# Performance work log

Hardware: AMD Instinct MI355X
Metric: run time of the kernel (lower is better)

Reference implementation:

```python
import jax, jax.numpy as jnp
import numpy as np

B, S, D, H, HID = 8192, 16, 128, 8, 1024
DH = D // H  # 16
GCN, NUMF = 40, 103
EPS = 1e-5

def _make_pe():
    pos = np.arange(S, dtype=np.float64)[:, None]
    i = np.arange(D, dtype=np.float64)[None, :]
    pe = pos / np.power(10000.0, (i // 2 * 2.0) / D)
    pe[:, 0::2] = np.sin(pe[:, 0::2])
    pe[:, 1::2] = np.cos(pe[:, 1::2])
    return jnp.asarray(pe, dtype=jnp.float32)  # [S, D]

PE = _make_pe()

def setup_inputs() -> dict:
    key = jax.random.key(0)
    ks = jax.random.split(key, 16)
    rn = lambda k, shape, s=0.02: (jax.random.normal(k, shape, jnp.float32) * s)
    return {
        "x": jax.random.normal(ks[0], (B, S, D), jnp.float32),
        "gcn_i": jax.random.normal(ks[1], (B, GCN), jnp.float32),
        "num": jax.random.normal(ks[2], (B, NUMF), jnp.float32),
        # two independent encoder layers, params stacked on leading dim
        "Wq": rn(ks[3], (2, D, D)), "bq": jnp.zeros((2, D), jnp.float32),
        "Wk": rn(ks[4], (2, D, D)), "bk": jnp.zeros((2, D), jnp.float32),
        "Wv": rn(ks[5], (2, D, D)), "bv": jnp.zeros((2, D), jnp.float32),
        "Wo": rn(ks[6], (2, D, D)), "bo": jnp.zeros((2, D), jnp.float32),
        "ln1_g": jnp.ones((2, D), jnp.float32), "ln1_b": jnp.zeros((2, D), jnp.float32),
        "W1": rn(ks[7], (2, D, HID)), "b1": jnp.zeros((2, HID), jnp.float32),
        "W2": rn(ks[8], (2, HID, D)), "b2": jnp.zeros((2, D), jnp.float32),
        "ln2_g": jnp.ones((2, D), jnp.float32), "ln2_b": jnp.zeros((2, D), jnp.float32),
        # head
        "Wn": rn(ks[9], (NUMF, D)), "bnum": jnp.zeros((D,), jnp.float32),
        "bn_gamma": jnp.ones((D,), jnp.float32), "bn_beta": jnp.zeros((D,), jnp.float32),
        "Wf": rn(ks[10], (S * D + GCN + D, 1)), "bf": jnp.zeros((1,), jnp.float32),
    }

def _ln(x, g, b):
    m = x.mean(-1, keepdims=True)
    v = ((x - m) ** 2).mean(-1, keepdims=True)
    return (x - m) * jax.lax.rsqrt(v + EPS) * g + b

def reference(x, gcn_i, num, Wq, bq, Wk, bk, Wv, bv, Wo, bo, ln1_g, ln1_b,
              W1, b1, W2, b2, ln2_g, ln2_b, Wn, bnum, bn_gamma, bn_beta, Wf, bf):
    out = x + PE  # positional encoding (dropout = identity in eval)
    scale = DH ** -0.5
    for l in range(2):
        # NOTE: original uses a raw .view(B*H, -1, DH) (no transpose) -- faithful reshape
        q = (out @ Wq[l] + bq[l]).reshape(B * H, S, DH)
        k = (out @ Wk[l] + bk[l]).reshape(B * H, S, DH)
        v = (out @ Wv[l] + bv[l]).reshape(B * H, S, DH)
        attn = jax.nn.softmax(jnp.einsum('nsd,ntd->nst', q, k) * scale, axis=-1)
        ctx = jnp.einsum('nst,ntd->nsd', attn, v).reshape(B, S, D)
        h = _ln(ctx @ Wo[l] + bo[l] + out, ln1_g[l], ln1_b[l])
        ff = jax.nn.relu(h @ W1[l] + b1[l]) @ W2[l] + b2[l]
        out = _ln(ff + h, ln2_g[l], ln2_b[l])
    flat = out.reshape(B, S * D)  # [B, 2048]
    n = num @ Wn + bnum  # [B, 128]
    # BatchNorm1d, training-mode forward (biased batch variance)
    mu = n.mean(0)
    var = ((n - mu) ** 2).mean(0)
    n = (n - mu) * jax.lax.rsqrt(var + EPS) * bn_gamma + bn_beta
    p = jnp.concatenate([flat, gcn_i, n], axis=-1)  # [B, 2216]
    return jax.nn.sigmoid(p @ Wf + bf)
```

## Files before the change

### kernel.cpp

```cpp
#include <hip/hip_runtime.h>
#include <hip/hip_bf16.h>
#include <math.h>

#define B_SZ   8192
#define S_SZ   16
#define D_SZ   128
#define HID_SZ 1024
#define NUMF_SZ 103
#define GCN_SZ 40
#define G_B    4
#define NBLK   (B_SZ / G_B)
#define SBLK   512
#define STRD   136

typedef short bh8 __attribute__((ext_vector_type(8)));
typedef float fx4 __attribute__((ext_vector_type(4)));
typedef unsigned short us4 __attribute__((ext_vector_type(4)));

__device__ __forceinline__ fx4 mfma16(bh8 a, bh8 b, fx4 c) {
    return __builtin_amdgcn_mfma_f32_16x16x32_bf16(a, b, c, 0, 0, 0);
}

__device__ __forceinline__ unsigned short f2b(float f) {
    union { __hip_bfloat16 b; unsigned short u; } cv;
    cv.b = __float2bfloat16(f);
    return cv.u;
}
__device__ __forceinline__ float bu2f(unsigned short u) {
    return __uint_as_float(((unsigned)u) << 16);
}

__global__ __launch_bounds__(256) void prep_weights(
    const float* __restrict__ Wq, const float* __restrict__ Wk,
    const float* __restrict__ Wv, const float* __restrict__ Wo,
    const float* __restrict__ W1, const float* __restrict__ W2,
    unsigned short* __restrict__ WswQ, unsigned short* __restrict__ WswK,
    unsigned short* __restrict__ WswV, unsigned short* __restrict__ WswO,
    unsigned short* __restrict__ Wsw1, unsigned short* __restrict__ Wsw2,
    float* __restrict__ PEt)
{
    int j = blockIdx.x * 256 + threadIdx.x;
    if (j < 2048) {
        int s = j >> 7, c = j & 127;
        float expo = (float)((c >> 1) * 2) * (1.0f / 128.0f);
        float denom = powf(10000.0f, expo);
        float ang = (float)s / denom;
        PEt[j] = (c & 1) ? cosf(ang) : sinf(ang);
    }
    if (j < 2 * 16384) {
        int r = j & 16383, l = j >> 14;
        int k = r >> 7, n = r & 127;
        int dst = (((l * 8 + (n >> 4)) * 4 + (k >> 5)) * 64 +
                   (((k >> 3) & 3) * 16 + (n & 15))) * 8 + (k & 7);
        WswQ[dst] = f2b(Wq[j]); WswK[dst] = f2b(Wk[j]);
        WswV[dst] = f2b(Wv[j]); WswO[dst] = f2b(Wo[j]);
    }
    {
        int l = j >> 17, r = j & 131071;
        int k = r >> 10, n = r & 1023;
        int dst = (((l * 64 + (n >> 4)) * 4 + (k >> 5)) * 64 +
                   (((k >> 3) & 3) * 16 + (n & 15))) * 8 + (k & 7);
        Wsw1[dst] = f2b(W1[j]);
    }
    {
        int l = j >> 17, r = j & 131071;
        int k = r >> 7, n = r & 127;
        int dst = (((l * 8 + (n >> 4)) * 32 + (k >> 5)) * 64 +
                   (((k >> 3) & 3) * 16 + (n & 15))) * 8 + (k & 7);
        Wsw2[dst] = f2b(W2[j]);
    }
}

__global__ __launch_bounds__(256, 2) void encoder_fused(
    const float* __restrict__ x, const float* __restrict__ gcn,
    const float* __restrict__ bq, const float* __restrict__ bk,
    const float* __restrict__ bv, const float* __restrict__ bo,
    const float* __restrict__ ln1g, const float* __restrict__ ln1b,
    const float* __restrict__ b1, const float* __restrict__ b2p,
    const float* __restrict__ ln2g, const float* __restrict__ ln2b,
    const float* __restrict__ Wf,
    const unsigned short* __restrict__ WswQ, const unsigned short* __restrict__ WswK,
    const unsigned short* __restrict__ WswV, const unsigned short* __restrict__ WswO,
    const unsigned short* __restrict__ Wsw1, const unsigned short* __restrict__ Wsw2,
    const float* __restrict__ PEt,
    const float* __restrict__ num, const float* __restrict__ Wn,
    const float* __restrict__ bnum,
    float* __restrict__ ssum, float* __restrict__ ssq,
    unsigned int* __restrict__ cnt,
    const float* __restrict__ bng, const float* __restrict__ bnb,
    const float* __restrict__ bfin, float* __restrict__ cvec,
    float* __restrict__ acc1)
{
    __shared__ unsigned short ACT[64][STRD];
    __shared__ unsigned short Qb[64][STRD];
    __shared__ unsigned short Kb[64][STRD];
    __shared__ unsigned short Vb[64][STRD];
    __shared__ float2 LNp2[64][4];
    __shared__ unsigned short Pb[4][16][16];
    __shared__ int lastf;

    unsigned short* Vb4 = &Vb[0][0];

    const int t = threadIdx.x;
    const int w = t >> 6, lane = t & 63;
    const int q = lane >> 4, ln = lane & 15;

    if (blockIdx.x < SBLK) {
        float* NUMs = (float*)ACT;
        float* cred = (float*)Qb;
        float* cS   = (float*)Vb;
        float* redw = (float*)LNp2;
        const int b0 = blockIdx.x * 16;
        const int j = t & 127, sg = t >> 7, s0 = sg * 8;

        for (int idx = t; idx < 16 * NUMF_SZ; idx += 256) {
            int r = idx / NUMF_SZ, f = idx - r * NUMF_SZ;
            NUMs[r * 104 + f] = num[(size_t)(b0 + r) * NUMF_SZ + f];
        }
        __syncthreads();

        float acc[8];
        float bnv = bnum[j];
#pragma unroll
        for (int r = 0; r < 8; ++r) acc[r] = bnv;
        for (int f = 0; f < NUMF_SZ; ++f) {
            float wv = Wn[f * 128 + j];
#pragma unroll
            for (int r = 0; r < 8; ++r) acc[r] = fmaf(NUMs[(s0 + r) * 104 + f], wv, acc[r]);
        }
        float lsum = 0.f, lsq = 0.f;
#pragma unroll
        for (int r = 0; r < 8; ++r) {
            lsum += acc[r];
            lsq = fmaf(acc[r], acc[r], lsq);
        }
        cred[sg * 128 + j] = lsum;
        cred[(2 + sg) * 128 + j] = lsq;
        __syncthreads();
        if (sg == 0) atomicAdd(&ssum[j], cred[j] + cred[128 + j]);
        else         atomicAdd(&ssq[j],  cred[256 + j] + cred[384 + j]);
        __syncthreads();
        if (t == 0) lastf = (atomicAdd(cnt, 1u) == SBLK - 1u) ? 1 : 0;
        __syncthreads();

        if (lastf) {
            float C1p = 0.f;
            if (t < 128) {
                float sv = atomicAdd(&ssum[t], 0.f);
                float qv = atomicAdd(&ssq[t], 0.f);
                float mean = sv * (1.0f / (float)B_SZ);
                float var = qv * (1.0f / (float)B_SZ) - mean * mean;
                float inv = rsqrtf(var + 1e-5f);
                float wj = Wf[2088 + t];
                float gi = bng[t] * inv;
                float cj = gi * wj;
                cS[t] = cj;
                C1p = (bnb[t] - mean * gi) * wj + bnum[t] * cj;
            }
#pragma unroll
            for (int o = 32; o; o >>= 1) C1p += __shfl_xor(C1p, o);
            if (lane == 0) redw[w] = C1p;
            __syncthreads();
            if (t == 0) cvec[103] = redw[0] + redw[1] + redw[2] + redw[3] + bfin[0];
            if (t < NUMF_SZ) {
                float s2 = 0.f;
                for (int jj = 0; jj < 128; ++jj)
                    s2 = fmaf(Wn[t * 128 + jj], cS[jj], s2);
                cvec[t] = s2;
            }
        }
        return;
    }

    const int bbase = (blockIdx.x - SBLK) * G_B;

    {
        const float4* xb = (const float4*)(x + (size_t)bbase * 2048);
        const float4* pe4 = (const float4*)PEt;
#pragma unroll
        for (int i = 0; i < 8; ++i) {
            int f4 = i * 256 + t;
            float4 xv = xb[f4];
            float4 pv = pe4[f4 & 511];
            int flat = f4 * 4;
            int row = flat >> 7, col = flat & 127;
            ushort4 pk = {f2b(xv.x + pv.x), f2b(xv.y + pv.y),
                          f2b(xv.z + pv.z), f2b(xv.w + pv.w)};
            *(ushort4*)&ACT[row][col] = pk;
        }
    }
    __syncthreads();

    for (int l = 0; l < 2; ++l) {
        {
            bh8 afr[4][4];
#pragma unroll
            for (int mt = 0; mt < 4; ++mt)
#pragma unroll
                for (int ks = 0; ks < 4; ++ks)
                    afr[mt][ks] = *(const bh8*)&ACT[mt * 16 + ln][ks * 32 + q * 8];
#pragma unroll
            for (int mtx = 0; mtx < 2; ++mtx) {
                const unsigned short* Wm = (mtx == 0) ? WswQ + l * 16384 : WswK + l * 16384;
                const float* bias = (mtx == 0) ? bq + l * 128 : bk + l * 128;
                unsigned short (*dst)[STRD] = (mtx == 0) ? Qb : Kb;
#pragma unroll
                for (int i2 = 0; i2 < 2; ++i2) {
                    int nt = w * 2 + i2;
                    bh8 wfr[4];
#pragma unroll
                    for (int ks = 0; ks < 4; ++ks)
                        wfr[ks] = *(const bh8*)(Wm + ((nt * 4 + ks) * 64 + lane) * 8);
                    int n0 = nt * 16 + q * 4;
                    fx4 bb4 = *(const fx4*)&bias[n0];
#pragma unroll
                    for (int mt = 0; mt < 4; ++mt) {
                        fx4 acc = {0.f, 0.f, 0.f, 0.f};
#pragma unroll
                        for (int ks = 0; ks < 4; ++ks) acc = mfma16(wfr[ks], afr[mt][ks], acc);
                        us4 o;
#pragma unroll
                        for (int r2 = 0; r2 < 4; ++r2) o[r2] = f2b(acc[r2] + bb4[r2]);
                        *(us4*)&dst[mt * 16 + ln][n0] = o;
                    }
                }
            }
#pragma unroll
            for (int i2 = 0; i2 < 2; ++i2) {
                int nt = w * 2 + i2;
                bh8 wfr[4];
#pragma unroll
                for (int ks = 0; ks < 4; ++ks)
                    wfr[ks] = *(const bh8*)(WswV + l * 16384 + ((nt * 4 + ks) * 64 + lane) * 8);
                int n = nt * 16 + ln;
                float bb = bv[l * 128 + n];
#pragma unroll
                for (int mt = 0; mt < 4; ++mt) {
                    fx4 acc = {0.f, 0.f, 0.f, 0.f};
#pragma unroll
                    for (int ks = 0; ks < 4; ++ks) acc = mfma16(afr[mt][ks], wfr[ks], acc);
#pragma unroll
                    for (int r2 = 0; r2 < 4; ++r2) {
                        int s = q * 4 + r2;
                        Vb4[(((mt * 8 + (s >> 1)) * 16) + ln) * 16 +
                            (((s & 1) << 3) | nt)] = f2b(acc[r2] + bb);
                    }
                }
            }
        }
        __syncthreads();

        {
            const int E = w;
            const int rbase = E * 16 + (ln >> 3);
            const int ccol = (ln & 7) * 16;
#pragma unroll
            for (int g = 0; g < 8; ++g) {
                bh8 kfr = 0, qfr = 0;
                if (q < 2) {
                    kfr = *(const bh8*)&Kb[rbase + 2 * g][ccol + q * 8];
                    qfr = *(const bh8*)&Qb[rbase + 2 * g][ccol + q * 8];
                }
                fx4 st = mfma16(kfr, qfr, fx4{0.f, 0.f, 0.f, 0.f});
                float p0 = st[0] * 0.25f, p1 = st[1] * 0.25f;
                float p2 = st[2] * 0.25f, p3 = st[3] * 0.25f;
                float mx = fmaxf(fmaxf(p0, p1), fmaxf(p2, p3));
                mx = fmaxf(mx, __shfl_xor(mx, 16));
                mx = fmaxf(mx, __shfl_xor(mx, 32));
                p0 = __expf(p0 - mx); p1 = __expf(p1 - mx);
                p2 = __expf(p2 - mx); p3 = __expf(p3 - mx);
                float sm = (p0 + p1) + (p2 + p3);
                sm += __shfl_xor(sm, 16);
                sm += __shfl_xor(sm, 32);
                float is = 1.0f / sm;
                ushort4 pk = {f2b(p0 * is), f2b(p1 * is), f2b(p2 * is), f2b(p3 * is)};
                *(ushort4*)&Pb[w][ln][q * 4] = pk;
                bh8 vfr = 0, pfr = 0;
                if (q < 2) {
                    vfr = *(const bh8*)&Vb4[(((E * 8 + g) * 16) + ln) * 16 + q * 8];
                    pfr = *(const bh8*)&Pb[w][ln][q * 8];
                }
                fx4 cx = mfma16(vfr, pfr, fx4{0.f, 0.f, 0.f, 0.f});
                ushort4 ck = {f2b(cx[0]), f2b(cx[1]), f2b(cx[2]), f2b(cx[3])};
                *(ushort4*)&Qb[rbase + 2 * g][ccol + q * 4] = ck;
            }
        }
        __syncthreads();

        fx4 Cv[2][4];
        {
            bh8 cfr[4][4];
#pragma unroll
            for (int mt = 0; mt < 4; ++mt)
#pragma unroll
                for (int ks = 0; ks < 4; ++ks)
                    cfr[mt][ks] = *(const bh8*)&Qb[mt * 16 + ln][ks * 32 + q * 8];
#pragma unroll
            for (int i2 = 0; i2 < 2; ++i2) {
                int nt = w * 2 + i2, n0 = nt * 16 + q * 4;
                bh8 wfr[4];
#pragma unroll
                for (int ks = 0; ks < 4; ++ks)
                    wfr[ks] = *(const bh8*)(WswO + l * 16384 + ((nt * 4 + ks) * 64 + lane) * 8);
                fx4 bb4 = *(const fx4*)&bo[l * 128 + n0];
#pragma unroll
                for (int mt = 0; mt < 4; ++mt) {
                    fx4 acc = {0.f, 0.f, 0.f, 0.f};
#pragma unroll
                    for (int ks = 0; ks < 4; ++ks) acc = mfma16(wfr[ks], cfr[mt][ks], acc);
                    us4 rv = *(const us4*)&ACT[mt * 16 + ln][n0];
#pragma unroll
                    for (int r2 = 0; r2 < 4; ++r2)
                        Cv[i2][mt][r2] = acc[r2] + bb4[r2] + bu2f(rv[r2]);
                }
            }
        }
#pragma unroll
        for (int mt = 0; mt < 4; ++mt) {
            float s = 0.f, v = 0.f;
#pragma unroll
            for (int i2 = 0; i2 < 2; ++i2)
#pragma unroll
                for (int r2 = 0; r2 < 4; ++r2) {
                    float a = Cv[i2][mt][r2];
                    s += a; v = fmaf(a, a, v);
                }
            s += __shfl_xor(s, 16); v += __shfl_xor(v, 16);
            s += __shfl_xor(s, 32); v += __shfl_xor(v, 32);
            if (lane < 16) LNp2[mt * 16 + ln][w] = float2{s, v};
        }
        __syncthreads();
        {
            float mean4[4], inv4[4];
#pragma unroll
            for (int mt = 0; mt < 4; ++mt) {
                int row = mt * 16 + ln;
                float2 a0 = LNp2[row][0], a1 = LNp2[row][1];
                float2 a2 = LNp2[row][2], a3 = LNp2[row][3];
                float s = (a0.x + a1.x) + (a2.x + a3.x);
                float v = (a0.y + a1.y) + (a2.y + a3.y);
                float mean = s * (1.0f / 128.0f);
                mean4[mt] = mean;
                inv4[mt] = rsqrtf(v * (1.0f / 128.0f) - mean * mean + 1e-5f);
            }
#pragma unroll
            for (int i2 = 0; i2 < 2; ++i2) {
                int n0 = (w * 2 + i2) * 16 + q * 4;
                fx4 gg = *(const fx4*)&ln1g[l * 128 + n0];
                fx4 be = *(const fx4*)&ln1b[l * 128 + n0];
#pragma unroll
                for (int mt = 0; mt < 4; ++mt) {
                    us4 o;
#pragma unroll
                    for (int r2 = 0; r2 < 4; ++r2)
                        o[r2] = f2b((Cv[i2][mt][r2] - mean4[mt]) * inv4[mt] * gg[r2] + be[r2]);
                    *(us4*)&Kb[mt * 16 + ln][n0] = o;
                }
            }
        }
        __syncthreads();

        bh8 hfr[4][4];
#pragma unroll
        for (int mt = 0; mt < 4; ++mt)
#pragma unroll
            for (int ks = 0; ks < 4; ++ks)
                hfr[mt][ks] = *(const bh8*)&Kb[mt * 16 + ln][ks * 32 + q * 8];
        fx4 f2a[2][4];
#pragma unroll
        for (int i2 = 0; i2 < 2; ++i2)
#pragma unroll
            for (int mt = 0; mt < 4; ++mt) f2a[i2][mt] = fx4{0.f, 0.f, 0.f, 0.f};
        for (int ch = 0; ch < 8; ++ch) {
            unsigned short (*dst)[STRD] = (ch & 1) ? Vb : Qb;
            bh8 w1fr[2][4];
#pragma unroll
            for (int i2 = 0; i2 < 2; ++i2) {
                int ntg = ch * 8 + w * 2 + i2;
#pragma unroll
                for (int ks = 0; ks < 4; ++ks)
                    w1fr[i2][ks] = *(const bh8*)(Wsw1 + l * 131072 + ((ntg * 4 + ks) * 64 + lane) * 8);
            }
#pragma unroll
            for (int mt = 0; mt < 4; ++mt) {
#pragma unroll
                for (int i2 = 0; i2 < 2; ++i2) {
                    fx4 acc = {0.f, 0.f, 0.f, 0.f};
#pragma unroll
                    for (int ks = 0; ks < 4; ++ks) acc = mfma16(w1fr[i2][ks], hfr[mt][ks], acc);
                    int nl0 = (w * 2 + i2) * 16 + q * 4;
                    fx4 bb4 = *(const fx4*)&b1[l * HID_SZ + ch * 128 + nl0];
                    us4 o;
#pragma unroll
                    for (int r2 = 0; r2 < 4; ++r2) {
                        float vv = acc[r2] + bb4[r2];
                        o[r2] = f2b(vv > 0.f ? vv : 0.f);
                    }
                    *(us4*)&dst[mt * 16 + ln][nl0] = o;
                }
            }
            __syncthreads();
            bh8 w2fr[2][4];
#pragma unroll
            for (int i2 = 0; i2 < 2; ++i2)
#pragma unroll
                for (int ks = 0; ks < 4; ++ks)
                    w2fr[i2][ks] = *(const bh8*)(Wsw2 + l * 131072 +
                        (((w * 2 + i2) * 32 + ch * 4 + ks) * 64 + lane) * 8);
#pragma unroll
            for (int mt = 0; mt < 4; ++mt) {
                bh8 ffr[4];
#pragma unroll
                for (int ks = 0; ks < 4; ++ks)
                    ffr[ks] = *(const bh8*)&dst[mt * 16 + ln][ks * 32 + q * 8];
#pragma unroll
                for (int i2 = 0; i2 < 2; ++i2)
#pragma unroll
                    for (int ks = 0; ks < 4; ++ks)
                        f2a[i2][mt] = mfma16(w2fr[i2][ks], ffr[ks], f2a[i2][mt]);
            }
        }
        fx4 Cv2[2][4];
#pragma unroll
        for (int i2 = 0; i2 < 2; ++i2) {
            int n0 = (w * 2 + i2) * 16 + q * 4;
            fx4 bb4 = *(const fx4*)&b2p[l * 128 + n0];
#pragma unroll
            for (int mt = 0; mt < 4; ++mt) {
                us4 rv = *(const us4*)&Kb[mt * 16 + ln][n0];
#pragma unroll
                for (int r2 = 0; r2 < 4; ++r2)
                    Cv2[i2][mt][r2] = f2a[i2][mt][r2] + bb4[r2] + bu2f(rv[r2]);
            }
        }
#pragma unroll
        for (int mt = 0; mt < 4; ++mt) {
            float s = 0.f, v = 0.f;
#pragma unroll
            for (int i2 = 0; i2 < 2; ++i2)
#pragma unroll
                for (int r2 = 0; r2 < 4; ++r2) {
                    float a = Cv2[i2][mt][r2];
                    s += a; v = fmaf(a, a, v);
                }
            s += __shfl_xor(s, 16); v += __shfl_xor(v, 16);
            s += __shfl_xor(s, 32); v += __shfl_xor(v, 32);
            if (lane < 16) LNp2[mt * 16 + ln][w] = float2{s, v};
        }
        __syncthreads();
        {
            float mean4[4], inv4[4];
#pragma unroll
            for (int mt = 0; mt < 4; ++mt) {
                int row = mt * 16 + ln;
                float2 a0 = LNp2[row][0], a1 = LNp2[row][1];
                float2 a2 = LNp2[row][2], a3 = LNp2[row][3];
                float s = (a0.x + a1.x) + (a2.x + a3.x);
                float v = (a0.y + a1.y) + (a2.y + a3.y);
                float mean = s * (1.0f / 128.0f);
                mean4[mt] = mean;
                inv4[mt] = rsqrtf(v * (1.0f / 128.0f) - mean * mean + 1e-5f);
            }
#pragma unroll
            for (int i2 = 0; i2 < 2; ++i2) {
                int n0 = (w * 2 + i2) * 16 + q * 4;
                fx4 gg = *(const fx4*)&ln2g[l * 128 + n0];
                fx4 be = *(const fx4*)&ln2b[l * 128 + n0];
#pragma unroll
                for (int mt = 0; mt < 4; ++mt) {
                    us4 o;
#pragma unroll
                    for (int r2 = 0; r2 < 4; ++r2)
                        o[r2] = f2b((Cv2[i2][mt][r2] - mean4[mt]) * inv4[mt] * gg[r2] + be[r2]);
                    *(us4*)&ACT[mt * 16 + ln][n0] = o;
                }
            }
        }
        __syncthreads();
    }

    {
        int bg = bbase + w;
        float part = 0.f;
        int srow = lane >> 2, c0 = (lane & 3) * 32;
#pragma unroll
        for (int i = 0; i < 4; ++i) {
            bh8 av = *(const bh8*)&ACT[w * 16 + srow][c0 + i * 8];
            int fl = srow * 128 + c0 + i * 8;
#pragma unroll
            for (int e = 0; e < 8; ++e)
                part = fmaf(bu2f((unsigned short)av[e]), Wf[fl + e], part);
        }
        if (lane < GCN_SZ)
            part = fmaf(gcn[(size_t)bg * GCN_SZ + lane], Wf[2048 + lane], part);
#pragma unroll
        for (int off = 32; off; off >>= 1) part += __shfl_xor(part, off);
        if (lane == 0) acc1[bg] = part;
    }
}

__global__ __launch_bounds__(256) void final_fast(
    const float* __restrict__ num, const float* __restrict__ cvec,
    const float* __restrict__ acc1, float* __restrict__ out)
{
    __shared__ float wv[104];
    const int t = threadIdx.x;
    if (t < 104) wv[t] = cvec[t];
    __syncthreads();
    const int w = t >> 6, lane = t & 63;
    const int b = blockIdx.x * 4 + w;
    const float* nb = num + (size_t)b * NUMF_SZ;
    float part = nb[lane] * wv[lane];
    if (lane < NUMF_SZ - 64) part += nb[64 + lane] * wv[64 + lane];
#pragma unroll
    for (int o = 32; o; o >>= 1) part += __shfl_xor(part, o);
    if (lane == 0)
        out[b] = 1.0f / (1.0f + __expf(-(acc1[b] + part + wv[103])));
}

extern "C" void kernel_launch(void* const* d_in, const int* in_sizes, int n_in,
                              void* d_out, int out_size, void* d_ws, size_t ws_size,
                              hipStream_t stream)
{
    const float* x    = (const float*)d_in[0];
    const float* gcn  = (const float*)d_in[1];
    const float* num  = (const float*)d_in[2];
    const float* Wq   = (const float*)d_in[3];
    const float* bq   = (const float*)d_in[4];
    const float* Wk   = (const float*)d_in[5];
    const float* bk   = (const float*)d_in[6];
    const float* Wv   = (const float*)d_in[7];
    const float* bv   = (const float*)d_in[8];
    const float* Wo   = (const float*)d_in[9];
    const float* bo   = (const float*)d_in[10];
    const float* ln1g = (const float*)d_in[11];
    const float* ln1b = (const float*)d_in[12];
    const float* W1   = (const float*)d_in[13];
    const float* b1   = (const float*)d_in[14];
    const float* W2   = (const float*)d_in[15];
    const float* b2p  = (const float*)d_in[16];
    const float* ln2g = (const float*)d_in[17];
    const float* ln2b = (const float*)d_in[18];
    const float* Wn   = (const float*)d_in[19];
    const float* bnum = (const float*)d_in[20];
    const float* bng  = (const float*)d_in[21];
    const float* bnb  = (const float*)d_in[22];
    const float* Wf   = (const float*)d_in[23];
    const float* bfin = (const float*)d_in[24];

    float* acc1 = (float*)d_ws;
    float* ssum = acc1 + B_SZ;
    float* ssq  = ssum + 128;
    unsigned int* cnt = (unsigned int*)(ssq + 128);
    unsigned short* wb = (unsigned short*)((char*)d_ws + 40960);
    unsigned short* WswQ = wb;
    unsigned short* WswK = wb + 32768;
    unsigned short* WswV = wb + 65536;
    unsigned short* WswO = wb + 98304;
    unsigned short* Wsw1 = wb + 131072;
    unsigned short* Wsw2 = wb + 393216;
    float* PEt = (float*)((char*)d_ws + 40960 + 1310720);
    float* cvec = (float*)((char*)d_ws + 40960 + 1310720 + 8192);

    hipMemsetAsync(ssum, 0, 257 * sizeof(float), stream);
    prep_weights<<<1024, 256, 0, stream>>>(Wq, Wk, Wv, Wo, W1, W2,
        WswQ, WswK, WswV, WswO, Wsw1, Wsw2, PEt);
    encoder_fused<<<SBLK + NBLK, 256, 0, stream>>>(x, gcn, bq, bk, bv, bo,
        ln1g, ln1b, b1, b2p, ln2g, ln2b, Wf,
        WswQ, WswK, WswV, WswO, Wsw1, Wsw2, PEt,
        num, Wn, bnum, ssum, ssq, cnt, bng, bnb, bfin, cvec, acc1);
    final_fast<<<B_SZ / 4, 256, 0, stream>>>(num, cvec, acc1, (float*)d_out);
}
```

Baseline: 403.8 us.

## Use 512-thread blocks with one output tile per wave in encoder kernel

Doubles the encoder block to 8 waves, so each wave owns one 16-column N-tile instead of two. Per-thread register arrays (weight fragments, accumulators, FFN hidden fragments) shrink, and launch bounds now request 4 blocks of 512 per CU. The stats blocks move after the encoder blocks in the grid, and the shared scratch arrays are unioned into one buffer. More waves give more latency hiding, at the cost of duplicated A-fragment LDS reads per wave and finer split work in attention and the final reduction.

```diff
diff --git a/kernel.cpp b/kernel.cpp
--- a/kernel.cpp
+++ b/kernel.cpp
@@ -71,7 +71,7 @@
     }
 }
 
-__global__ __launch_bounds__(256, 2) void encoder_fused(
+__global__ __launch_bounds__(512, 4) void encoder_fused(
     const float* __restrict__ x, const float* __restrict__ gcn,
     const float* __restrict__ bq, const float* __restrict__ bk,
     const float* __restrict__ bv, const float* __restrict__ bo,
@@ -95,50 +95,53 @@
     __shared__ unsigned short Qb[64][STRD];
     __shared__ unsigned short Kb[64][STRD];
     __shared__ unsigned short Vb[64][STRD];
-    __shared__ float2 LNp2[64][4];
-    __shared__ unsigned short Pb[4][16][16];
+    __shared__ unsigned long long SCRU[512];
     __shared__ int lastf;
 
-    unsigned short* Vb4 = &Vb[0][0];
+    unsigned short* Pb   = (unsigned short*)SCRU;
+    float2*         LNp2 = (float2*)SCRU;
+    float*          redw = (float*)SCRU;
+    unsigned short* Vb4  = &Vb[0][0];
 
     const int t = threadIdx.x;
     const int w = t >> 6, lane = t & 63;
     const int q = lane >> 4, ln = lane & 15;
 
-    if (blockIdx.x < SBLK) {
+    if (blockIdx.x >= NBLK) {
         float* NUMs = (float*)ACT;
         float* cred = (float*)Qb;
         float* cS   = (float*)Vb;
-        float* redw = (float*)LNp2;
-        const int b0 = blockIdx.x * 16;
-        const int j = t & 127, sg = t >> 7, s0 = sg * 8;
-
-        for (int idx = t; idx < 16 * NUMF_SZ; idx += 256) {
+        const int b0 = (blockIdx.x - NBLK) * 16;
+        const int j = t & 127, sg = t >> 7, s0 = sg * 4;
+
+        for (int idx = t; idx < 16 * NUMF_SZ; idx += 512) {
             int r = idx / NUMF_SZ, f = idx - r * NUMF_SZ;
             NUMs[r * 104 + f] = num[(size_t)(b0 + r) * NUMF_SZ + f];
         }
         __syncthreads();
 
-        float acc[8];
+        float acc[4];
         float bnv = bnum[j];
 #pragma unroll
-        for (int r = 0; r < 8; ++r) acc[r] = bnv;
+        for (int r = 0; r < 4; ++r) acc[r] = bnv;
         for (int f = 0; f < NUMF_SZ; ++f) {
             float wv = Wn[f * 128 + j];
 #pragma unroll
-            for (int r = 0; r < 8; ++r) acc[r] = fmaf(NUMs[(s0 + r) * 104 + f], wv, acc[r]);
+            for (int r = 0; r < 4; ++r) acc[r] = fmaf(NUMs[(s0 + r) * 104 + f], wv, acc[r]);
         }
         float lsum = 0.f, lsq = 0.f;
 #pragma unroll
-        for (int r = 0; r < 8; ++r) {
+        for (int r = 0; r < 4; ++r) {
             lsum += acc[r];
             lsq = fmaf(acc[r], acc[r], lsq);
         }
         cred[sg * 128 + j] = lsum;
-        cred[(2 + sg) * 128 + j] = lsq;
-        __syncthreads();
-        if (sg == 0) atomicAdd(&ssum[j], cred[j] + cred[128 + j]);
-        else         atomicAdd(&ssq[j],  cred[256 + j] + cred[384 + j]);
+        cred[(4 + sg) * 128 + j] = lsq;
+        __syncthreads();
+        if (sg == 0) atomicAdd(&ssum[j], (cred[j] + cred[128 + j]) +
+                                         (cred[256 + j] + cred[384 + j]));
+        else if (sg == 1) atomicAdd(&ssq[j], (cred[512 + j] + cred[640 + j]) +
+                                             (cred[768 + j] + cred[896 + j]));
         __syncthreads();
         if (t == 0) lastf = (atomicAdd(cnt, 1u) == SBLK - 1u) ? 1 : 0;
         __syncthreads();
@@ -161,7 +164,8 @@
             for (int o = 32; o; o >>= 1) C1p += __shfl_xor(C1p, o);
             if (lane == 0) redw[w] = C1p;
             __syncthreads();
-            if (t == 0) cvec[103] = redw[0] + redw[1] + redw[2] + redw[3] + bfin[0];
+            if (t == 0) cvec[103] = ((redw[0] + redw[1]) + (redw[2] + redw[3])) +
+                                    ((redw[4] + redw[5]) + (redw[6] + redw[7])) + bfin[0];
             if (t < NUMF_SZ) {
                 float s2 = 0.f;
                 for (int jj = 0; jj < 128; ++jj)
@@ -172,14 +176,15 @@
         return;
     }
 
-    const int bbase = (blockIdx.x - SBLK) * G_B;
+    const int bbase = blockIdx.x * G_B;
+    const int n0 = w * 16 + q * 4;
 
     {
         const float4* xb = (const float4*)(x + (size_t)bbase * 2048);
         const float4* pe4 = (const float4*)PEt;
 #pragma unroll
-        for (int i = 0; i < 8; ++i) {
-            int f4 = i * 256 + t;
+        for (int i = 0; i < 4; ++i) {
+            int f4 = i * 512 + t;
             float4 xv = xb[f4];
             float4 pv = pe4[f4 & 511];
             int flat = f4 * 4;
@@ -204,35 +209,28 @@
                 const unsigned short* Wm = (mtx == 0) ? WswQ + l * 16384 : WswK + l * 16384;
                 const float* bias = (mtx == 0) ? bq + l * 128 : bk + l * 128;
                 unsigned short (*dst)[STRD] = (mtx == 0) ? Qb : Kb;
-#pragma unroll
-                for (int i2 = 0; i2 < 2; ++i2) {
-                    int nt = w * 2 + i2;
-                    bh8 wfr[4];
-#pragma unroll
-                    for (int ks = 0; ks < 4; ++ks)
-                        wfr[ks] = *(const bh8*)(Wm + ((nt * 4 + ks) * 64 + lane) * 8);
-                    int n0 = nt * 16 + q * 4;
-                    fx4 bb4 = *(const fx4*)&bias[n0];
-#pragma unroll
-                    for (int mt = 0; mt < 4; ++mt) {
-                        fx4 acc = {0.f, 0.f, 0.f, 0.f};
-#pragma unroll
-                        for (int ks = 0; ks < 4; ++ks) acc = mfma16(wfr[ks], afr[mt][ks], acc);
-                        us4 o;
-#pragma unroll
-                        for (int r2 = 0; r2 < 4; ++r2) o[r2] = f2b(acc[r2] + bb4[r2]);
-                        *(us4*)&dst[mt * 16 + ln][n0] = o;
-                    }
-                }
-            }
-#pragma unroll
-            for (int i2 = 0; i2 < 2; ++i2) {
-                int nt = w * 2 + i2;
                 bh8 wfr[4];
 #pragma unroll
                 for (int ks = 0; ks < 4; ++ks)
-                    wfr[ks] = *(const bh8*)(WswV + l * 16384 + ((nt * 4 + ks) * 64 + lane) * 8);
-                int n = nt * 16 + ln;
+                    wfr[ks] = *(const bh8*)(Wm + ((w * 4 + ks) * 64 + lane) * 8);
+                fx4 bb4 = *(const fx4*)&bias[n0];
+#pragma unroll
+                for (int mt = 0; mt < 4; ++mt) {
+                    fx4 acc = {0.f, 0.f, 0.f, 0.f};
+#pragma unroll
+                    for (int ks = 0; ks < 4; ++ks) acc = mfma16(wfr[ks], afr[mt][ks], acc);
+                    us4 o;
+#pragma unroll
+                    for (int r2 = 0; r2 < 4; ++r2) o[r2] = f2b(acc[r2] + bb4[r2]);
+                    *(us4*)&dst[mt * 16 + ln][n0] = o;
+                }
+            }
+            {
+                bh8 wfr[4];
+#pragma unroll
+                for (int ks = 0; ks < 4; ++ks)
+                    wfr[ks] = *(const bh8*)(WswV + l * 16384 + ((w * 4 + ks) * 64 + lane) * 8);
+                int n = w * 16 + ln;
                 float bb = bv[l * 128 + n];
 #pragma unroll
                 for (int mt = 0; mt < 4; ++mt) {
@@ -243,7 +241,7 @@
                     for (int r2 = 0; r2 < 4; ++r2) {
                         int s = q * 4 + r2;
                         Vb4[(((mt * 8 + (s >> 1)) * 16) + ln) * 16 +
-                            (((s & 1) << 3) | nt)] = f2b(acc[r2] + bb);
+                            (((s & 1) << 3) | w)] = f2b(acc[r2] + bb);
                     }
                 }
             }
@@ -251,11 +249,13 @@
         __syncthreads();
 
         {
-            const int E = w;
-            const int rbase = E * 16 + (ln >> 3);
+            const int e = w >> 1;
+            const int g4 = (w & 1) * 4;
+            const int rbase = e * 16 + (ln >> 3);
             const int ccol = (ln & 7) * 16;
 #pragma unroll
-            for (int g = 0; g < 8; ++g) {
+            for (int g2 = 0; g2 < 4; ++g2) {
+                int g = g4 + g2;
                 bh8 kfr = 0, qfr = 0;
                 if (q < 2) {
                     kfr = *(const bh8*)&Kb[rbase + 2 * g][ccol + q * 8];
@@ -274,11 +274,11 @@
                 sm += __shfl_xor(sm, 32);
                 float is = 1.0f / sm;
                 ushort4 pk = {f2b(p0 * is), f2b(p1 * is), f2b(p2 * is), f2b(p3 * is)};
-                *(ushort4*)&Pb[w][ln][q * 4] = pk;
+                *(ushort4*)&Pb[(w * 16 + ln) * 16 + q * 4] = pk;
                 bh8 vfr = 0, pfr = 0;
                 if (q < 2) {
-                    vfr = *(const bh8*)&Vb4[(((E * 8 + g) * 16) + ln) * 16 + q * 8];
-                    pfr = *(const bh8*)&Pb[w][ln][q * 8];
+                    vfr = *(const bh8*)&Vb4[(((e * 8 + g) * 16) + ln) * 16 + q * 8];
+                    pfr = *(const bh8*)&Pb[(w * 16 + ln) * 16 + q * 8];
                 }
                 fx4 cx = mfma16(vfr, pfr, fx4{0.f, 0.f, 0.f, 0.f});
                 ushort4 ck = {f2b(cx[0]), f2b(cx[1]), f2b(cx[2]), f2b(cx[3])};
@@ -287,7 +287,7 @@
         }
         __syncthreads();
 
-        fx4 Cv[2][4];
+        fx4 Cv[4];
         {
             bh8 cfr[4][4];
 #pragma unroll
@@ -295,39 +295,33 @@
 #pragma unroll
                 for (int ks = 0; ks < 4; ++ks)
                     cfr[mt][ks] = *(const bh8*)&Qb[mt * 16 + ln][ks * 32 + q * 8];
-#pragma unroll
-            for (int i2 = 0; i2 < 2; ++i2) {
-                int nt = w * 2 + i2, n0 = nt * 16 + q * 4;
-                bh8 wfr[4];
-#pragma unroll
-                for (int ks = 0; ks < 4; ++ks)
-                    wfr[ks] = *(const bh8*)(WswO + l * 16384 + ((nt * 4 + ks) * 64 + lane) * 8);
-                fx4 bb4 = *(const fx4*)&bo[l * 128 + n0];
-#pragma unroll
-                for (int mt = 0; mt < 4; ++mt) {
-                    fx4 acc = {0.f, 0.f, 0.f, 0.f};
-#pragma unroll
-                    for (int ks = 0; ks < 4; ++ks) acc = mfma16(wfr[ks], cfr[mt][ks], acc);
-                    us4 rv = *(const us4*)&ACT[mt * 16 + ln][n0];
-#pragma unroll
-                    for (int r2 = 0; r2 < 4; ++r2)
-                        Cv[i2][mt][r2] = acc[r2] + bb4[r2] + bu2f(rv[r2]);
-                }
+            bh8 wfr[4];
+#pragma unroll
+            for (int ks = 0; ks < 4; ++ks)
+                wfr[ks] = *(const bh8*)(WswO + l * 16384 + ((w * 4 + ks) * 64 + lane) * 8);
+            fx4 bb4 = *(const fx4*)&bo[l * 128 + n0];
+#pragma unroll
+            for (int mt = 0; mt < 4; ++mt) {
+                fx4 acc = {0.f, 0.f, 0.f, 0.f};
+#pragma unroll
+                for (int ks = 0; ks < 4; ++ks) acc = mfma16(wfr[ks], cfr[mt][ks], acc);
+                us4 rv = *(const us4*)&ACT[mt * 16 + ln][n0];
+#pragma unroll
+                for (int r2 = 0; r2 < 4; ++r2)
+                    Cv[mt][r2] = acc[r2] + bb4[r2] + bu2f(rv[r2]);
             }
         }
 #pragma unroll
         for (int mt = 0; mt < 4; ++mt) {
             float s = 0.f, v = 0.f;
 #pragma unroll
-            for (int i2 = 0; i2 < 2; ++i2)
-#pragma unroll
-                for (int r2 = 0; r2 < 4; ++r2) {
-                    float a = Cv[i2][mt][r2];
-                    s += a; v = fmaf(a, a, v);
-                }
+            for (int r2 = 0; r2 < 4; ++r2) {
+                float a = Cv[mt][r2];
+                s += a; v = fmaf(a, a, v);
+            }
             s += __shfl_xor(s, 16); v += __shfl_xor(v, 16);
             s += __shfl_xor(s, 32); v += __shfl_xor(v, 32);
-            if (lane < 16) LNp2[mt * 16 + ln][w] = float2{s, v};
+            if (lane < 16) LNp2[(mt * 16 + ln) * 8 + w] = float2{s, v};
         }
         __syncthreads();
         {
@@ -335,78 +329,63 @@
 #pragma unroll
             for (int mt = 0; mt < 4; ++mt) {
                 int row = mt * 16 + ln;
-                float2 a0 = LNp2[row][0], a1 = LNp2[row][1];
-                float2 a2 = LNp2[row][2], a3 = LNp2[row][3];
-                float s = (a0.x + a1.x) + (a2.x + a3.x);
-                float v = (a0.y + a1.y) + (a2.y + a3.y);
+                float s = 0.f, v = 0.f;
+#pragma unroll
+                for (int ww = 0; ww < 8; ++ww) {
+                    float2 a = LNp2[row * 8 + ww];
+                    s += a.x; v += a.y;
+                }
                 float mean = s * (1.0f / 128.0f);
                 mean4[mt] = mean;
                 inv4[mt] = rsqrtf(v * (1.0f / 128.0f) - mean * mean + 1e-5f);
             }
-#pragma unroll
-            for (int i2 = 0; i2 < 2; ++i2) {
-                int n0 = (w * 2 + i2) * 16 + q * 4;
-                fx4 gg = *(const fx4*)&ln1g[l * 128 + n0];
-                fx4 be = *(const fx4*)&ln1b[l * 128 + n0];
-#pragma unroll
-                for (int mt = 0; mt < 4; ++mt) {
-                    us4 o;
-#pragma unroll
-                    for (int r2 = 0; r2 < 4; ++r2)
-                        o[r2] = f2b((Cv[i2][mt][r2] - mean4[mt]) * inv4[mt] * gg[r2] + be[r2]);
-                    *(us4*)&Kb[mt * 16 + ln][n0] = o;
-                }
-            }
-        }
-        __syncthreads();
-
-        bh8 hfr[4][4];
-#pragma unroll
-        for (int mt = 0; mt < 4; ++mt)
-#pragma unroll
-            for (int ks = 0; ks < 4; ++ks)
-                hfr[mt][ks] = *(const bh8*)&Kb[mt * 16 + ln][ks * 32 + q * 8];
-        fx4 f2a[2][4];
-#pragma unroll
-        for (int i2 = 0; i2 < 2; ++i2)
-#pragma unroll
-            for (int mt = 0; mt < 4; ++mt) f2a[i2][mt] = fx4{0.f, 0.f, 0.f, 0.f};
+            fx4 gg = *(const fx4*)&ln1g[l * 128 + n0];
+            fx4 be = *(const fx4*)&ln1b[l * 128 + n0];
+#pragma unroll
+            for (int mt = 0; mt < 4; ++mt) {
+                us4 o;
+#pragma unroll
+                for (int r2 = 0; r2 < 4; ++r2)
+                    o[r2] = f2b((Cv[mt][r2] - mean4[mt]) * inv4[mt] * gg[r2] + be[r2]);
+                *(us4*)&Kb[mt * 16 + ln][n0] = o;
+            }
+        }
+        __syncthreads();
+
+        fx4 f2a[4];
+#pragma unroll
+        for (int mt = 0; mt < 4; ++mt) f2a[mt] = fx4{0.f, 0.f, 0.f, 0.f};
         for (int ch = 0; ch < 8; ++ch) {
             unsigned short (*dst)[STRD] = (ch & 1) ? Vb : Qb;
-            bh8 w1fr[2][4];
-#pragma unroll
-            for (int i2 = 0; i2 < 2; ++i2) {
-                int ntg = ch * 8 + w * 2 + i2;
-#pragma unroll
-                for (int ks = 0; ks < 4; ++ks)
-                    w1fr[i2][ks] = *(const bh8*)(Wsw1 + l * 131072 + ((ntg * 4 + ks) * 64 + lane) * 8);
-            }
-#pragma unroll
-            for (int mt = 0; mt < 4; ++mt) {
-#pragma unroll
-                for (int i2 = 0; i2 < 2; ++i2) {
-                    fx4 acc = {0.f, 0.f, 0.f, 0.f};
-#pragma unroll
-                    for (int ks = 0; ks < 4; ++ks) acc = mfma16(w1fr[i2][ks], hfr[mt][ks], acc);
-                    int nl0 = (w * 2 + i2) * 16 + q * 4;
-                    fx4 bb4 = *(const fx4*)&b1[l * HID_SZ + ch * 128 + nl0];
-                    us4 o;
-#pragma unroll
-                    for (int r2 = 0; r2 < 4; ++r2) {
-                        float vv = acc[r2] + bb4[r2];
-                        o[r2] = f2b(vv > 0.f ? vv : 0.f);
-                    }
-                    *(us4*)&dst[mt * 16 + ln][nl0] = o;
-                }
+            bh8 w1fr[4];
+            int ntg = ch * 8 + w;
+#pragma unroll
+            for (int ks = 0; ks < 4; ++ks)
+                w1fr[ks] = *(const bh8*)(Wsw1 + l * 131072 + ((ntg * 4 + ks) * 64 + lane) * 8);
+            fx4 bb4 = *(const fx4*)&b1[l * HID_SZ + ch * 128 + n0];
+#pragma unroll
+            for (int mt = 0; mt < 4; ++mt) {
+                bh8 hfr[4];
+#pragma unroll
+                for (int ks = 0; ks < 4; ++ks)
+                    hfr[ks] = *(const bh8*)&Kb[mt * 16 + ln][ks * 32 + q * 8];
+                fx4 acc = {0.f, 0.f, 0.f, 0.f};
+#pragma unroll
+                for (int ks = 0; ks < 4; ++ks) acc = mfma16(w1fr[ks], hfr[ks], acc);
+                us4 o;
+#pragma unroll
+                for (int r2 = 0; r2 < 4; ++r2) {
+                    float vv = acc[r2] + bb4[r2];
+                    o[r2] = f2b(vv > 0.f ? vv : 0.f);
+                }
+                *(us4*)&dst[mt * 16 + ln][n0] = o;
             }
             __syncthreads();
-            bh8 w2fr[2][4];
-#pragma unroll
-            for (int i2 = 0; i2 < 2; ++i2)
-#pragma unroll
-                for (int ks = 0; ks < 4; ++ks)
-                    w2fr[i2][ks] = *(const bh8*)(Wsw2 + l * 131072 +
-                        (((w * 2 + i2) * 32 + ch * 4 + ks) * 64 + lane) * 8);
+            bh8 w2fr[4];
+#pragma unroll
+            for (int ks = 0; ks < 4; ++ks)
+                w2fr[ks] = *(const bh8*)(Wsw2 + l * 131072 +
+                    ((w * 32 + ch * 4 + ks) * 64 + lane) * 8);
 #pragma unroll
             for (int mt = 0; mt < 4; ++mt) {
                 bh8 ffr[4];
@@ -414,38 +393,32 @@
                 for (int ks = 0; ks < 4; ++ks)
                     ffr[ks] = *(const bh8*)&dst[mt * 16 + ln][ks * 32 + q * 8];
 #pragma unroll
-                for (int i2 = 0; i2 < 2; ++i2)
-#pragma unroll
-                    for (int ks = 0; ks < 4; ++ks)
-                        f2a[i2][mt] = mfma16(w2fr[i2][ks], ffr[ks], f2a[i2][mt]);
-            }
-        }
-        fx4 Cv2[2][4];
-#pragma unroll
-        for (int i2 = 0; i2 < 2; ++i2) {
-            int n0 = (w * 2 + i2) * 16 + q * 4;
+                for (int ks = 0; ks < 4; ++ks)
+                    f2a[mt] = mfma16(w2fr[ks], ffr[ks], f2a[mt]);
+            }
+        }
+        fx4 Cv2[4];
+        {
             fx4 bb4 = *(const fx4*)&b2p[l * 128 + n0];
 #pragma unroll
             for (int mt = 0; mt < 4; ++mt) {
                 us4 rv = *(const us4*)&Kb[mt * 16 + ln][n0];
 #pragma unroll
                 for (int r2 = 0; r2 < 4; ++r2)
-                    Cv2[i2][mt][r2] = f2a[i2][mt][r2] + bb4[r2] + bu2f(rv[r2]);
+                    Cv2[mt][r2] = f2a[mt][r2] + bb4[r2] + bu2f(rv[r2]);
             }
         }
 #pragma unroll
         for (int mt = 0; mt < 4; ++mt) {
             float s = 0.f, v = 0.f;
 #pragma unroll
-            for (int i2 = 0; i2 < 2; ++i2)
-#pragma unroll
-                for (int r2 = 0; r2 < 4; ++r2) {
-                    float a = Cv2[i2][mt][r2];
-                    s += a; v = fmaf(a, a, v);
-                }
+            for (int r2 = 0; r2 < 4; ++r2) {
+                float a = Cv2[mt][r2];
+                s += a; v = fmaf(a, a, v);
+            }
             s += __shfl_xor(s, 16); v += __shfl_xor(v, 16);
             s += __shfl_xor(s, 32); v += __shfl_xor(v, 32);
-            if (lane < 16) LNp2[mt * 16 + ln][w] = float2{s, v};
+            if (lane < 16) LNp2[(mt * 16 + ln) * 8 + w] = float2{s, v};
         }
         __syncthreads();
         {
@@ -453,50 +426,54 @@
 #pragma unroll
             for (int mt = 0; mt < 4; ++mt) {
                 int row = mt * 16 + ln;
-                float2 a0 = LNp2[row][0], a1 = LNp2[row][1];
-                float2 a2 = LNp2[row][2], a3 = LNp2[row][3];
-                float s = (a0.x + a1.x) + (a2.x + a3.x);
-                float v = (a0.y + a1.y) + (a2.y + a3.y);
+                float s = 0.f, v = 0.f;
+#pragma unroll
+                for (int ww = 0; ww < 8; ++ww) {
+                    float2 a = LNp2[row * 8 + ww];
+                    s += a.x; v += a.y;
+                }
                 float mean = s * (1.0f / 128.0f);
                 mean4[mt] = mean;
                 inv4[mt] = rsqrtf(v * (1.0f / 128.0f) - mean * mean + 1e-5f);
             }
-#pragma unroll
-            for (int i2 = 0; i2 < 2; ++i2) {
-                int n0 = (w * 2 + i2) * 16 + q * 4;
-                fx4 gg = *(const fx4*)&ln2g[l * 128 + n0];
-                fx4 be = *(const fx4*)&ln2b[l * 128 + n0];
-#pragma unroll
-                for (int mt = 0; mt < 4; ++mt) {
-                    us4 o;
-#pragma unroll
-                    for (int r2 = 0; r2 < 4; ++r2)
-                        o[r2] = f2b((Cv2[i2][mt][r2] - mean4[mt]) * inv4[mt] * gg[r2] + be[r2]);
-                    *(us4*)&ACT[mt * 16 + ln][n0] = o;
-                }
+            fx4 gg = *(const fx4*)&ln2g[l * 128 + n0];
+            fx4 be = *(const fx4*)&ln2b[l * 128 + n0];
+#pragma unroll
+            for (int mt = 0; mt < 4; ++mt) {
+                us4 o;
+#pragma unroll
+                for (int r2 = 0; r2 < 4; ++r2)
+                    o[r2] = f2b((Cv2[mt][r2] - mean4[mt]) * inv4[mt] * gg[r2] + be[r2]);
+                *(us4*)&ACT[mt * 16 + ln][n0] = o;
             }
         }
         __syncthreads();
     }
 
     {
-        int bg = bbase + w;
+        const int e = w >> 1, h2 = w & 1;
+        int bg = bbase + e;
         float part = 0.f;
-        int srow = lane >> 2, c0 = (lane & 3) * 32;
-#pragma unroll
-        for (int i = 0; i < 4; ++i) {
-            bh8 av = *(const bh8*)&ACT[w * 16 + srow][c0 + i * 8];
-            int fl = srow * 128 + c0 + i * 8;
-#pragma unroll
-            for (int e = 0; e < 8; ++e)
-                part = fmaf(bu2f((unsigned short)av[e]), Wf[fl + e], part);
-        }
-        if (lane < GCN_SZ)
-            part = fmaf(gcn[(size_t)bg * GCN_SZ + lane], Wf[2048 + lane], part);
+        int r = h2 * 8 + (lane >> 3), c0 = (lane & 7) * 16;
+#pragma unroll
+        for (int i = 0; i < 2; ++i) {
+            bh8 av = *(const bh8*)&ACT[e * 16 + r][c0 + i * 8];
+            int fl = r * 128 + c0 + i * 8;
+#pragma unroll
+            for (int e8 = 0; e8 < 8; ++e8)
+                part = fmaf(bu2f((unsigned short)av[e8]), Wf[fl + e8], part);
+        }
+        if (lane < 20) {
+            int gi = h2 * 20 + lane;
+            part = fmaf(gcn[(size_t)bg * GCN_SZ + gi], Wf[2048 + gi], part);
+        }
 #pragma unroll
         for (int off = 32; off; off >>= 1) part += __shfl_xor(part, off);
-        if (lane == 0) acc1[bg] = part;
-    }
+        if (lane == 0) redw[w] = part;
+    }
+    __syncthreads();
+    if (t < G_B)
+        acc1[bbase + t] = redw[2 * t] + redw[2 * t + 1];
 }
 
 __global__ __launch_bounds__(256) void final_fast(
@@ -565,7 +542,7 @@
     hipMemsetAsync(ssum, 0, 257 * sizeof(float), stream);
     prep_weights<<<1024, 256, 0, stream>>>(Wq, Wk, Wv, Wo, W1, W2,
         WswQ, WswK, WswV, WswO, Wsw1, Wsw2, PEt);
-    encoder_fused<<<SBLK + NBLK, 256, 0, stream>>>(x, gcn, bq, bk, bv, bo,
+    encoder_fused<<<NBLK + SBLK, 512, 0, stream>>>(x, gcn, bq, bk, bv, bo,
         ln1g, ln1b, b1, b2p, ln2g, ln2b, Wf,
         WswQ, WswK, WswV, WswO, Wsw1, Wsw2, PEt,
         num, Wn, bnum, ssum, ssq, cnt, bng, bnb, bfin, cvec, acc1);
```

Result: slower. 440.0 us (+9.0%).
